# Kernel optimization log

Measured on AMD Instinct MI355X. Metric: run time of the kernel, lower is better.

## Reference

```python
import jax, jax.numpy as jnp
import numpy as np
import math

DIM = 384
HEADS = 12
WIN = (12, 12)
N = WIN[0] * WIN[1]  # 144
TABLE = (2 * WIN[0] - 1) * (2 * WIN[1] - 1)  # 529
B_ = 512
NW = 16
CPB_HIDDEN = 512


def setup_inputs() -> dict:
    key = jax.random.key(0)
    ks = jax.random.split(key, 12)
    x = jax.random.normal(ks[0], (B_, N, DIM), dtype=jnp.float32)
    relative_coords_table = jax.random.uniform(ks[1], (1, 2 * WIN[0] - 1, 2 * WIN[1] - 1, 2), dtype=jnp.float32) * 2.0 - 1.0
    relative_position_index = jax.random.randint(ks[2], (N, N), 0, TABLE, dtype=jnp.int64)
    mask = jnp.zeros((NW, N, N), dtype=jnp.float32)
    # learned params
    qkv_w = jax.random.normal(ks[3], (3 * DIM, DIM), dtype=jnp.float32) * (1.0 / math.sqrt(DIM))
    q_bias = jnp.zeros((DIM,), dtype=jnp.float32)
    k_bias = jnp.zeros((DIM,), dtype=jnp.float32)
    v_bias = jnp.zeros((DIM,), dtype=jnp.float32)
    logit_scale = jnp.full((HEADS, 1, 1), math.log(10.0), dtype=jnp.float32)
    cpb_w1 = jax.random.normal(ks[4], (CPB_HIDDEN, 2), dtype=jnp.float32) * 0.5
    cpb_b1 = jnp.zeros((CPB_HIDDEN,), dtype=jnp.float32)
    cpb_w2 = jax.random.normal(ks[5], (HEADS, CPB_HIDDEN), dtype=jnp.float32) * (1.0 / math.sqrt(CPB_HIDDEN))
    proj_w = jax.random.normal(ks[6], (DIM, DIM), dtype=jnp.float32) * (1.0 / math.sqrt(DIM))
    proj_b = jnp.zeros((DIM,), dtype=jnp.float32)
    return {
        'x': x,
        'relative_coords_table': relative_coords_table,
        'relative_position_index': relative_position_index,
        'mask': mask,
        'qkv_w': qkv_w, 'q_bias': q_bias, 'k_bias': k_bias, 'v_bias': v_bias,
        'logit_scale': logit_scale,
        'cpb_w1': cpb_w1, 'cpb_b1': cpb_b1, 'cpb_w2': cpb_w2,
        'proj_w': proj_w, 'proj_b': proj_b,
    }


def reference(x, relative_coords_table, relative_position_index, mask,
              qkv_w, q_bias, k_bias, v_bias, logit_scale,
              cpb_w1, cpb_b1, cpb_w2, proj_w, proj_b):
    Bw, n, C = x.shape
    H = HEADS
    d = C // H
    qkv_bias = jnp.concatenate([q_bias, k_bias, v_bias])
    qkv = x @ qkv_w.T + qkv_bias  # (Bw, n, 3C)
    qkv = qkv.reshape(Bw, n, 3, H, d).transpose(2, 0, 3, 1, 4)  # (3, Bw, H, n, d)
    q, k, v = qkv[0], qkv[1], qkv[2]
    # cosine attention
    qn = q / jnp.linalg.norm(q, axis=-1, keepdims=True)
    kn = k / jnp.linalg.norm(k, axis=-1, keepdims=True)
    attn = jnp.einsum('bhnd,bhmd->bhnm', qn, kn)
    scale = jnp.exp(jnp.minimum(logit_scale, math.log(1.0 / 0.01)))  # (H,1,1)
    attn = attn * scale[None]
    # CPB-MLP relative position bias
    h1 = jax.nn.relu(relative_coords_table @ cpb_w1.T + cpb_b1)  # (1,23,23,512)
    table = (h1 @ cpb_w2.T).reshape(-1, H)  # (529, H)
    rpb = table[relative_position_index.reshape(-1)].reshape(n, n, H)
    rpb = 16.0 * jax.nn.sigmoid(rpb.transpose(2, 0, 1))  # (H, n, n)
    attn = attn + rpb[None]
    # shifted-window mask
    nW = mask.shape[0]
    attn = attn.reshape(Bw // nW, nW, H, n, n) + mask[None, :, None]
    attn = attn.reshape(Bw, H, n, n)
    attn = jax.nn.softmax(attn, axis=-1)
    out = jnp.einsum('bhnm,bhmd->bhnd', attn, v)
    out = out.transpose(0, 2, 1, 3).reshape(Bw, n, C)
    out = out @ proj_w.T + proj_b
    return out
```

## Files before the change

### kernel.cpp

```cpp
#include <hip/hip_runtime.h>

#define DIMC 384
#define NHEADS 12
#define NTOK 144
#define TABLEN 529
#define BWIN 512
#define NWIN 16
#define CPBH 512

typedef unsigned short u16;
typedef unsigned int u32;
typedef __attribute__((ext_vector_type(8))) short short8;
typedef __attribute__((ext_vector_type(4))) float f32x4;

#define MFMA(a, b, c) __builtin_amdgcn_mfma_f32_16x16x32_bf16((a), (b), (c), 0, 0, 0)

__device__ __forceinline__ u16 f2bf(float f) {
  union { float f; u32 u; } v; v.f = f;
  u32 r = v.u + 0x7fffu + ((v.u >> 16) & 1u);
  return (u16)(r >> 16);
}
__device__ __forceinline__ u32 pk2(float a, float b) {
  return (u32)f2bf(a) | ((u32)f2bf(b) << 16);
}
__device__ __forceinline__ int swz4(int r) { return (r ^ (r >> 2)) & 3; }

__global__ __launch_bounds__(256) void cvt_bf16(const float* __restrict__ in,
                                                u16* __restrict__ out, int n8) {
  int i = blockIdx.x * 256 + threadIdx.x;
  if (i >= n8) return;
  const float4* p = (const float4*)(in + (size_t)i * 8);
  float4 a = p[0], b = p[1];
  uint4 r;
  r.x = pk2(a.x, a.y); r.y = pk2(a.z, a.w);
  r.z = pk2(b.x, b.y); r.w = pk2(b.z, b.w);
  *(uint4*)(out + (size_t)i * 8) = r;
}

__global__ void cpb_kernel(const float* __restrict__ rct,
                           const float* __restrict__ w1,
                           const float* __restrict__ b1,
                           const float* __restrict__ w2,
                           const float* __restrict__ logit_scale,
                           float* __restrict__ bias_tab,
                           float* __restrict__ scalev) {
  int t = blockIdx.x * blockDim.x + threadIdx.x;
  if (t < NHEADS) scalev[t] = __expf(fminf(logit_scale[t], 4.60517018598809f));
  if (t >= TABLEN * NHEADS) return;
  int i = t / NHEADS, h = t % NHEADS;
  float c0 = rct[2 * i], c1 = rct[2 * i + 1];
  const float* w2h = w2 + (size_t)h * CPBH;
  float acc = 0.f;
  for (int k = 0; k < CPBH; ++k) {
    float hv = fmaxf(0.f, fmaf(c0, w1[2 * k], fmaf(c1, w1[2 * k + 1], b1[k])));
    acc = fmaf(hv, w2h[k], acc);
  }
  bias_tab[i * NHEADS + h] = 16.f / (1.f + __expf(-acc));
}

__global__ __launch_bounds__(256) void cbias_kernel(const int* __restrict__ rpi,
                                                    const float* __restrict__ bias_tab,
                                                    const float* __restrict__ mask,
                                                    float* __restrict__ cb) {
  int e = blockIdx.x * 256 + threadIdx.x;
  if (e >= NWIN * NHEADS * NTOK * NTOK) return;
  int m = e % NTOK;
  int t = e / NTOK;
  int n = t % NTOK; t /= NTOK;
  int h = t % NHEADS;
  int w = t / NHEADS;
  cb[e] = bias_tab[rpi[n * NTOK + m] * NHEADS + h] + mask[(w * NTOK + n) * NTOK + m];
}

__global__ __launch_bounds__(576) void attn_fused(
    const u16* __restrict__ xb, const u16* __restrict__ wb,
    const float* __restrict__ q_bias, const float* __restrict__ k_bias,
    const float* __restrict__ v_bias, const float* __restrict__ cb,
    const float* __restrict__ scalev, u16* __restrict__ ctx) {
  __shared__ u16 smem[22656];
  u16* qn = smem;
  u16* kn = smem + 5760;
  u16* vT = smem + 11520;
  u16* Pc = smem + 16896;
  u16* xs = smem;
  u16* wsm = smem + 4608;

  int bid = blockIdx.x;
  int xcd = bid & 7;
  int i = bid >> 3;
  int wsub = i / 384;
  int j = i - wsub * 384;
  int bI = j / NHEADS;
  int h = j - bI * NHEADS;
  int w = xcd * 2 + wsub;
  int b = bI * NWIN + w;

  int tid = threadIdx.x;
  int lane = tid & 63, wv = tid >> 6;
  int g = lane >> 4, c = lane & 15;
  int rbase = wv * 16;

  f32x4 acc[6];
#pragma unroll
  for (int d = 0; d < 6; ++d) acc[d] = (f32x4){0.f, 0.f, 0.f, 0.f};

  int r4 = tid >> 2, b4 = tid & 3;
  bool hasW = tid < 384;
  int wrow = (r4 >> 5) * DIMC + h * 32 + (r4 & 31);
  int xwo = r4 * 32 + 8 * (b4 ^ swz4(r4));

  uint4 px, pw;
  px = *(const uint4*)(xb + ((size_t)b * NTOK + r4) * DIMC + b4 * 8);
  if (hasW) pw = *(const uint4*)(wb + (size_t)wrow * DIMC + b4 * 8);

  for (int t = 0; t < 12; ++t) {
    *(uint4*)(xs + xwo) = px;
    if (hasW) *(uint4*)(wsm + xwo) = pw;
    __syncthreads();
    if (t < 11) {
      int k0 = (t + 1) * 32;
      px = *(const uint4*)(xb + ((size_t)b * NTOK + r4) * DIMC + k0 + b4 * 8);
      if (hasW) pw = *(const uint4*)(wb + (size_t)wrow * DIMC + k0 + b4 * 8);
    }
    int arow = rbase + c;
    short8 ax = *(const short8*)(xs + arow * 32 + 8 * (g ^ swz4(arow)));
#pragma unroll
    for (int ni = 0; ni < 6; ++ni) {
      int row = ni * 16 + c;
      short8 bw = *(const short8*)(wsm + row * 32 + 8 * (g ^ swz4(row)));
      acc[ni] = MFMA(ax, bw, acc[ni]);
    }
    __syncthreads();
  }

  float sch = scalev[h];
  float qb0 = q_bias[h * 32 + c], qb1 = q_bias[h * 32 + 16 + c];
  float kb0 = k_bias[h * 32 + c], kb1 = k_bias[h * 32 + 16 + c];
  float vb0 = v_bias[h * 32 + c], vb1 = v_bias[h * 32 + 16 + c];
#pragma unroll
  for (int r = 0; r < 4; ++r) {
    int row = rbase + g * 4 + r;
    float q0 = acc[0][r] + qb0, q1 = acc[1][r] + qb1;
    float ssq = q0 * q0 + q1 * q1;
    ssq += __shfl_xor(ssq, 1); ssq += __shfl_xor(ssq, 2);
    ssq += __shfl_xor(ssq, 4); ssq += __shfl_xor(ssq, 8);
    float siq = sch / sqrtf(ssq);
    qn[row * 40 + c] = f2bf(q0 * siq);
    qn[row * 40 + 16 + c] = f2bf(q1 * siq);
    float k0v = acc[2][r] + kb0, k1v = acc[3][r] + kb1;
    float ssk = k0v * k0v + k1v * k1v;
    ssk += __shfl_xor(ssk, 1); ssk += __shfl_xor(ssk, 2);
    ssk += __shfl_xor(ssk, 4); ssk += __shfl_xor(ssk, 8);
    float sik = 1.f / sqrtf(ssk);
    kn[row * 40 + c] = f2bf(k0v * sik);
    kn[row * 40 + 16 + c] = f2bf(k1v * sik);
    float v0 = acc[4][r] + vb0;
    float v1 = acc[5][r] + vb1;
    vT[c * 168 + row] = f2bf(v0);
    vT[(16 + c) * 168 + row] = f2bf(v1);
  }
  if (tid < 32) {
    uint4 z4 = {0u, 0u, 0u, 0u};
    *(uint4*)(vT + tid * 168 + 144) = z4;
    *(uint4*)(vT + tid * 168 + 152) = z4;
    *(uint4*)(vT + tid * 168 + 160) = z4;
  }
  __syncthreads();

  short8 aq = *(const short8*)(qn + (rbase + c) * 40 + g * 8);
  f32x4 S[9];
#pragma unroll
  for (int mt = 0; mt < 9; ++mt) {
    short8 bk = *(const short8*)(kn + (mt * 16 + c) * 40 + g * 8);
    f32x4 z = (f32x4){0.f, 0.f, 0.f, 0.f};
    S[mt] = MFMA(aq, bk, z);
  }

  const float* cbh = cb + (((size_t)w * NHEADS + h) * NTOK) * NTOK;
#pragma unroll
  for (int r = 0; r < 4; ++r) {
    int row = rbase + g * 4 + r;
    const float* crow = cbh + (size_t)row * NTOK + c;
    float sv[9];
    float mx = -1e30f;
#pragma unroll
    for (int mt = 0; mt < 9; ++mt) {
      float s = S[mt][r] + crow[mt * 16];
      sv[mt] = s;
      mx = fmaxf(mx, s);
    }
    mx = fmaxf(mx, __shfl_xor(mx, 1)); mx = fmaxf(mx, __shfl_xor(mx, 2));
    mx = fmaxf(mx, __shfl_xor(mx, 4)); mx = fmaxf(mx, __shfl_xor(mx, 8));
    float sum = 0.f;
#pragma unroll
    for (int mt = 0; mt < 9; ++mt) {
      float p = __expf(sv[mt] - mx);
      sv[mt] = p;
      sum += p;
    }
    sum += __shfl_xor(sum, 1); sum += __shfl_xor(sum, 2);
    sum += __shfl_xor(sum, 4); sum += __shfl_xor(sum, 8);
    float rinv = 1.f / sum;
#pragma unroll
    for (int mt = 0; mt < 9; ++mt) S[mt][r] = sv[mt] * rinv;
  }

  f32x4 po[2];
  po[0] = (f32x4){0.f, 0.f, 0.f, 0.f};
  po[1] = (f32x4){0.f, 0.f, 0.f, 0.f};
  for (int ck = 0; ck < 5; ++ck) {
#pragma unroll
    for (int mt2 = 0; mt2 < 2; ++mt2) {
      int MT = ck * 2 + mt2;
#pragma unroll
      for (int r = 0; r < 4; ++r) {
        int row = rbase + g * 4 + r;
        float p = (MT < 9) ? S[MT][r] : 0.f;
        Pc[row * 40 + mt2 * 16 + c] = f2bf(p);
      }
    }
    short8 pa = *(const short8*)(Pc + (rbase + c) * 40 + g * 8);
#pragma unroll
    for (int dt = 0; dt < 2; ++dt) {
      short8 vb = *(const short8*)(vT + (dt * 16 + c) * 168 + ck * 32 + g * 8);
      po[dt] = MFMA(pa, vb, po[dt]);
    }
  }

#pragma unroll
  for (int dt = 0; dt < 2; ++dt)
#pragma unroll
    for (int r = 0; r < 4; ++r) {
      int n = rbase + g * 4 + r;
      ctx[((size_t)b * NTOK + n) * DIMC + h * 32 + dt * 16 + c] = f2bf(po[dt][r]);
    }
}

__global__ __launch_bounds__(256) void proj_gemm(const u16* __restrict__ ctx,
                                                 const u16* __restrict__ pwb,
                                                 const float* __restrict__ proj_b,
                                                 float* __restrict__ out) {
  __shared__ u16 As[128 * 64];
  __shared__ u16 Bs[128 * 64];
  int bid = blockIdx.x;
  int nblk = bid % 3, mblk = bid / 3;
  size_t gm0 = (size_t)mblk * 128;
  int gn0 = nblk * 128;
  int tid = threadIdx.x, lane = tid & 63, wid = tid >> 6;
  int wr = wid >> 1, wc = wid & 1, g = lane >> 4, c = lane & 15;
  f32x4 acc[4][4];
#pragma unroll
  for (int i = 0; i < 4; ++i)
#pragma unroll
    for (int j = 0; j < 4; ++j) acc[i][j] = (f32x4){0.f, 0.f, 0.f, 0.f};

  for (int t = 0; t < 6; ++t) {
    int k0 = t * 64;
#pragma unroll
    for (int p = 0; p < 4; ++p) {
      int row = p * 32 + (tid >> 3);
      int seg = (tid & 7) * 8;
      uint4 va = *(const uint4*)(ctx + (gm0 + row) * DIMC + k0 + seg);
      *(uint4*)(As + row * 64 + seg) = va;
      uint4 vb = *(const uint4*)(pwb + (size_t)(gn0 + row) * DIMC + k0 + seg);
      *(uint4*)(Bs + row * 64 + seg) = vb;
    }
    __syncthreads();
#pragma unroll
    for (int kk = 0; kk < 64; kk += 32) {
      short8 a[4], bfr[4];
#pragma unroll
      for (int mi = 0; mi < 4; ++mi)
        a[mi] = *(const short8*)(As + (wr * 64 + mi * 16 + c) * 64 + kk + g * 8);
#pragma unroll
      for (int ni = 0; ni < 4; ++ni)
        bfr[ni] = *(const short8*)(Bs + (wc * 64 + ni * 16 + c) * 64 + kk + g * 8);
#pragma unroll
      for (int mi = 0; mi < 4; ++mi)
#pragma unroll
        for (int ni = 0; ni < 4; ++ni)
          acc[mi][ni] = MFMA(a[mi], bfr[ni], acc[mi][ni]);
    }
    __syncthreads();
  }
#pragma unroll
  for (int mi = 0; mi < 4; ++mi)
#pragma unroll
    for (int ni = 0; ni < 4; ++ni) {
      int gcol = gn0 + wc * 64 + ni * 16 + c;
      float bv = proj_b[gcol];
#pragma unroll
      for (int r = 0; r < 4; ++r) {
        size_t grow = gm0 + wr * 64 + mi * 16 + g * 4 + r;
        out[grow * DIMC + gcol] = acc[mi][ni][r] + bv;
      }
    }
}

extern "C" void kernel_launch(void* const* d_in, const int* in_sizes, int n_in,
                              void* d_out, int out_size, void* d_ws, size_t ws_size,
                              hipStream_t stream) {
  const float* x = (const float*)d_in[0];
  const float* rct = (const float*)d_in[1];
  const int* rpi = (const int*)d_in[2];
  const float* mask = (const float*)d_in[3];
  const float* qkv_w = (const float*)d_in[4];
  const float* q_bias = (const float*)d_in[5];
  const float* k_bias = (const float*)d_in[6];
  const float* v_bias = (const float*)d_in[7];
  const float* logit_scale = (const float*)d_in[8];
  const float* cpb_w1 = (const float*)d_in[9];
  const float* cpb_b1 = (const float*)d_in[10];
  const float* cpb_w2 = (const float*)d_in[11];
  const float* proj_w = (const float*)d_in[12];
  const float* proj_b = (const float*)d_in[13];
  float* out = (float*)d_out;

  char* ws = (char*)d_ws;
  size_t off = 0;
  auto alloc = [&](size_t bytes) {
    void* p = ws + off;
    off = (off + bytes + 255) & ~(size_t)255;
    return p;
  };
  const size_t NX = (size_t)BWIN * NTOK * DIMC;
  u16* xb = (u16*)alloc(NX * 2);
  u16* wqb = (u16*)alloc((size_t)3 * DIMC * DIMC * 2);
  u16* pwb = (u16*)alloc((size_t)DIMC * DIMC * 2);
  u16* ctx = (u16*)alloc(NX * 2);
  float* cbv = (float*)alloc((size_t)NWIN * NHEADS * NTOK * NTOK * 4);
  float* bias_tab = (float*)alloc((size_t)TABLEN * NHEADS * 4);
  float* scalev = (float*)alloc(64 * 4);

  cvt_bf16<<<(int)(NX / 8 + 255) / 256, 256, 0, stream>>>(x, xb, (int)(NX / 8));
  cvt_bf16<<<(3 * DIMC * DIMC / 8 + 255) / 256, 256, 0, stream>>>(qkv_w, wqb, 3 * DIMC * DIMC / 8);
  cvt_bf16<<<(DIMC * DIMC / 8 + 255) / 256, 256, 0, stream>>>(proj_w, pwb, DIMC * DIMC / 8);
  cpb_kernel<<<(TABLEN * NHEADS + 255) / 256, 256, 0, stream>>>(
      rct, cpb_w1, cpb_b1, cpb_w2, logit_scale, bias_tab, scalev);
  cbias_kernel<<<(NWIN * NHEADS * NTOK * NTOK + 255) / 256, 256, 0, stream>>>(
      rpi, bias_tab, mask, cbv);
  attn_fused<<<BWIN * NHEADS, 576, 0, stream>>>(
      xb, wqb, q_bias, k_bias, v_bias, cbv, scalev, ctx);
  proj_gemm<<<(BWIN * NTOK / 128) * 3, 256, 0, stream>>>(ctx, pwb, proj_b, out);
}
```

Measured before the change: 367.0 us.

## Fuse x fp32-to-bf16 conversion into attention QKV load and widen K-tile to 64

The standalone kernel that converts x to bf16 is removed. The attention kernel now reads fp32 x directly and packs it to bf16 in registers with v_cvt_pk_bf16_f32 before storing to shared memory. The QKV K-loop goes from 12 steps of 32 to 6 steps of 64, with a new XOR swizzle and a larger shared-memory staging area, which halves the number of barriers. The cost is that each of the 12 head-blocks per window re-reads fp32 x, twice as many bytes as before, though L2 may absorb much of this. The packing instruction's rounding may also differ slightly from the old software rounding.

Result: slower. 437.4 us (+19.2%).

```diff
diff --git a/kernel.cpp b/kernel.cpp
--- a/kernel.cpp
+++ b/kernel.cpp
@@ -23,7 +23,11 @@
 __device__ __forceinline__ u32 pk2(float a, float b) {
   return (u32)f2bf(a) | ((u32)f2bf(b) << 16);
 }
-__device__ __forceinline__ int swz4(int r) { return (r ^ (r >> 2)) & 3; }
+__device__ __forceinline__ u32 cvtpk(float lo, float hi) {
+  u32 r;
+  asm("v_cvt_pk_bf16_f32 %0, %1, %2" : "=v"(r) : "v"(lo), "v"(hi));
+  return r;
+}
 
 __global__ __launch_bounds__(256) void cvt_bf16(const float* __restrict__ in,
                                                 u16* __restrict__ out, int n8) {
@@ -73,7 +77,7 @@
 }
 
 __global__ __launch_bounds__(576) void attn_fused(
-    const u16* __restrict__ xb, const u16* __restrict__ wb,
+    const float* __restrict__ x, const u16* __restrict__ wb,
     const float* __restrict__ q_bias, const float* __restrict__ k_bias,
     const float* __restrict__ v_bias, const float* __restrict__ cb,
     const float* __restrict__ scalev, u16* __restrict__ ctx) {
@@ -83,7 +87,7 @@
   u16* vT = smem + 11520;
   u16* Pc = smem + 16896;
   u16* xs = smem;
-  u16* wsm = smem + 4608;
+  u16* wsm = smem + 9216;
 
   int bid = blockIdx.x;
   int xcd = bid & 7;
@@ -104,31 +108,61 @@
 #pragma unroll
   for (int d = 0; d < 6; ++d) acc[d] = (f32x4){0.f, 0.f, 0.f, 0.f};
 
-  int r4 = tid >> 2, b4 = tid & 3;
-  bool hasW = tid < 384;
-  int wrow = (r4 >> 5) * DIMC + h * 32 + (r4 & 31);
-  int xwo = r4 * 32 + 8 * (b4 ^ swz4(r4));
-
-  uint4 px, pw;
-  px = *(const uint4*)(xb + ((size_t)b * NTOK + r4) * DIMC + b4 * 8);
-  if (hasW) pw = *(const uint4*)(wb + (size_t)wrow * DIMC + b4 * 8);
-
-  for (int t = 0; t < 12; ++t) {
-    *(uint4*)(xs + xwo) = px;
-    if (hasW) *(uint4*)(wsm + xwo) = pw;
+  int xr0 = tid >> 3, xk0 = tid & 7;
+  int xr1 = (tid + 576) >> 3, xk1 = tid & 7;
+  bool hasW2 = tid < 192;
+  int wr1 = (tid + 576) >> 3;
+  int wrowg0 = (xr0 >> 5) * DIMC + h * 32 + (xr0 & 31);
+  int wrowg1 = (wr1 >> 5) * DIMC + h * 32 + (wr1 & 31);
+  const float* xrow0 = x + ((size_t)b * NTOK + xr0) * DIMC + xk0 * 8;
+  const float* xrow1 = x + ((size_t)b * NTOK + xr1) * DIMC + xk1 * 8;
+  int xo0 = xr0 * 64 + 8 * (xk0 ^ (xr0 & 7));
+  int xo1 = xr1 * 64 + 8 * (xk1 ^ (xr1 & 7));
+  int wo0 = xr0 * 64 + 8 * (xk0 ^ (xr0 & 7));
+  int wr0 = tid >> 3;
+  int wk0 = tid & 7;
+  int wrowg0b = (wr0 >> 5) * DIMC + h * 32 + (wr0 & 31);
+  int woA = wr0 * 64 + 8 * (wk0 ^ (wr0 & 7));
+  int woB = wr1 * 64 + 8 * (xk1 ^ (wr1 & 7));
+
+  float4 pxa0, pxb0, pxa1, pxb1;
+  uint4 pw0, pw1;
+  {
+    pxa0 = *(const float4*)xrow0; pxb0 = *(const float4*)(xrow0 + 4);
+    pxa1 = *(const float4*)xrow1; pxb1 = *(const float4*)(xrow1 + 4);
+    pw0 = *(const uint4*)(wb + (size_t)wrowg0b * DIMC + wk0 * 8);
+    if (hasW2) pw1 = *(const uint4*)(wb + (size_t)wrowg1 * DIMC + xk1 * 8);
+  }
+
+  for (int t = 0; t < 6; ++t) {
+    {
+      uint4 v0 = (uint4){cvtpk(pxa0.x, pxa0.y), cvtpk(pxa0.z, pxa0.w),
+                         cvtpk(pxb0.x, pxb0.y), cvtpk(pxb0.z, pxb0.w)};
+      uint4 v1 = (uint4){cvtpk(pxa1.x, pxa1.y), cvtpk(pxa1.z, pxa1.w),
+                         cvtpk(pxb1.x, pxb1.y), cvtpk(pxb1.z, pxb1.w)};
+      *(uint4*)(xs + xo0) = v0;
+      *(uint4*)(xs + xo1) = v1;
+      *(uint4*)(wsm + woA) = pw0;
+      if (hasW2) *(uint4*)(wsm + woB) = pw1;
+    }
     __syncthreads();
-    if (t < 11) {
-      int k0 = (t + 1) * 32;
-      px = *(const uint4*)(xb + ((size_t)b * NTOK + r4) * DIMC + k0 + b4 * 8);
-      if (hasW) pw = *(const uint4*)(wb + (size_t)wrow * DIMC + k0 + b4 * 8);
+    if (t < 5) {
+      int k0 = (t + 1) * 64;
+      pxa0 = *(const float4*)(xrow0 + k0); pxb0 = *(const float4*)(xrow0 + k0 + 4);
+      pxa1 = *(const float4*)(xrow1 + k0); pxb1 = *(const float4*)(xrow1 + k0 + 4);
+      pw0 = *(const uint4*)(wb + (size_t)wrowg0b * DIMC + k0 + wk0 * 8);
+      if (hasW2) pw1 = *(const uint4*)(wb + (size_t)wrowg1 * DIMC + k0 + xk1 * 8);
     }
     int arow = rbase + c;
-    short8 ax = *(const short8*)(xs + arow * 32 + 8 * (g ^ swz4(arow)));
-#pragma unroll
-    for (int ni = 0; ni < 6; ++ni) {
-      int row = ni * 16 + c;
-      short8 bw = *(const short8*)(wsm + row * 32 + 8 * (g ^ swz4(row)));
-      acc[ni] = MFMA(ax, bw, acc[ni]);
+#pragma unroll
+    for (int kh = 0; kh < 2; ++kh) {
+      short8 ax = *(const short8*)(xs + arow * 64 + 8 * ((g + 4 * kh) ^ (c & 7)));
+#pragma unroll
+      for (int ni = 0; ni < 6; ++ni) {
+        int row = ni * 16 + c;
+        short8 bw = *(const short8*)(wsm + row * 64 + 8 * ((g + 4 * kh) ^ (c & 7)));
+        acc[ni] = MFMA(ax, bw, acc[ni]);
+      }
     }
     __syncthreads();
   }
@@ -324,7 +358,6 @@
     return p;
   };
   const size_t NX = (size_t)BWIN * NTOK * DIMC;
-  u16* xb = (u16*)alloc(NX * 2);
   u16* wqb = (u16*)alloc((size_t)3 * DIMC * DIMC * 2);
   u16* pwb = (u16*)alloc((size_t)DIMC * DIMC * 2);
   u16* ctx = (u16*)alloc(NX * 2);
@@ -332,7 +365,6 @@
   float* bias_tab = (float*)alloc((size_t)TABLEN * NHEADS * 4);
   float* scalev = (float*)alloc(64 * 4);
 
-  cvt_bf16<<<(int)(NX / 8 + 255) / 256, 256, 0, stream>>>(x, xb, (int)(NX / 8));
   cvt_bf16<<<(3 * DIMC * DIMC / 8 + 255) / 256, 256, 0, stream>>>(qkv_w, wqb, 3 * DIMC * DIMC / 8);
   cvt_bf16<<<(DIMC * DIMC / 8 + 255) / 256, 256, 0, stream>>>(proj_w, pwb, DIMC * DIMC / 8);
   cpb_kernel<<<(TABLEN * NHEADS + 255) / 256, 256, 0, stream>>>(
@@ -340,6 +372,6 @@
   cbias_kernel<<<(NWIN * NHEADS * NTOK * NTOK + 255) / 256, 256, 0, stream>>>(
       rpi, bias_tab, mask, cbv);
   attn_fused<<<BWIN * NHEADS, 576, 0, stream>>>(
-      xb, wqb, q_bias, k_bias, v_bias, cbv, scalev, ctx);
+      x, wqb, q_bias, k_bias, v_bias, cbv, scalev, ctx);
   proj_gemm<<<(BWIN * NTOK / 128) * 3, 256, 0, stream>>>(ctx, pwb, proj_b, out);
 }
```
